# Optimization experiments

Measured on AMD Instinct MI355X. Metric: run time of the kernel, lower is better.

## Reference

```python
import jax, jax.numpy as jnp
import numpy as np

EPS = 1e-12  # torch F.normalize eps


def setup_inputs() -> dict:
    key = jax.random.key(0)
    k1, k2, k3 = jax.random.split(key, 3)
    B, D, H, W, K = 64, 512, 32, 32, 64
    x = jax.random.normal(k1, (B, D, H, W), dtype=jnp.float32)
    w = jax.random.normal(k2, (K, D), dtype=jnp.float32) * 0.05  # 1x1 conv weight
    c = jax.random.normal(k3, (K, D), dtype=jnp.float32)          # cluster centers
    return {"x": x, "w": w, "c": c}


def reference(x, w, c):
    B, D, H, W = x.shape
    K = w.shape[0]
    N = H * W
    # 1x1 conv (no bias): (B,D,H,W) x (K,D) -> (B,K,H,W)
    features = jnp.einsum('bdhw,kd->bkhw', x, w)
    # NOTE: original applies softmax over dim=2 (the H axis only)
    a_bar = jax.nn.softmax(features, axis=2)
    xf = x.reshape(B, D, N)
    a = a_bar.reshape(B, K, N)
    # V[b,k,d] = sum_n a[b,k,n] * (x[b,d,n] - c[k,d])
    V = jnp.einsum('bkn,bdn->bkd', a, xf) - a.sum(axis=2)[:, :, None] * c[None]
    V = V.transpose(2, 1, 0)  # (D, K, B)
    # F.normalize(V, p=2, dim=1) applied twice (second is idempotent)
    norm = jnp.maximum(jnp.linalg.norm(V, axis=1, keepdims=True), EPS)
    y = V / norm
    norm2 = jnp.maximum(jnp.linalg.norm(y, axis=1, keepdims=True), EPS)
    return y / norm2
```

## Files before the change

kernel.cpp:

```cpp
#include <hip/hip_runtime.h>


typedef __attribute__((ext_vector_type(8))) short short8;
typedef __attribute__((ext_vector_type(4))) float f32x4;
typedef unsigned short u16;
typedef unsigned int u32;

union S8u { u32 q[4]; short8 s; };

__device__ __forceinline__ u32 pk2(float lo, float hi) {
  union { float f; u32 u; } a, b; a.f = lo; b.f = hi;
  u32 xl = (a.u + 0x7fffu + ((a.u >> 16) & 1u)) >> 16;
  u32 xh = (b.u + 0x7fffu + ((b.u >> 16) & 1u)) & 0xffff0000u;
  return xl | xh;
}

typedef const __attribute__((address_space(1))) u32 GU32;
typedef __attribute__((address_space(3))) u32 LU32;
__device__ __forceinline__ void glds16(const void* g, void* l) {
  __builtin_amdgcn_global_load_lds((GU32*)g, (LU32*)l, 16, 0, 0);
}

__global__ __launch_bounds__(256) void k0_packw(
    const float* __restrict__ w, u16* __restrict__ wsw)
{
  const int tg = blockIdx.x * 256 + threadIdx.x;
  const int dd4 = tg & 7, i = (tg >> 3) & 15, k = tg >> 7;
  f32x4 v = *(const f32x4*)(w + k * 512 + i * 32 + dd4 * 4);
  u32* dst = (u32*)(wsw + (size_t)(i * 64 + k) * 32 + dd4 * 4);
  dst[0] = pk2(v[0], v[1]);
  dst[1] = pk2(v[2], v[3]);
}

__global__ __launch_bounds__(256, 3) void k1_features(
    const float* __restrict__ x, const u16* __restrict__ wsw,
    float* __restrict__ feat)
{
  const int blk = blockIdx.x;
  const int b = blk & 63, nt = blk >> 6;
  const int nb = nt * 64;
  const int tid = threadIdx.x, lane = tid & 63, wv = tid >> 6;
  const int row = lane & 15, q = lane >> 4;

  __shared__ __align__(16) float xs[4][32][64];

  const char* xbase = (const char*)(x + ((size_t)b << 19) + nb);
  const int r0 = tid >> 4, cb = (tid & 15) * 16;

  f32x4 acc[4];
#pragma unroll
  for (int mt = 0; mt < 4; mt++) acc[mt] = (f32x4){0.f, 0.f, 0.f, 0.f};

  short8 wf[4][4];

#define STAGE1(s)                                                              \
  {                                                                            \
    char* lx = (char*)&xs[(s) & 3][0][0];                                      \
    const char* gx = xbase + (size_t)(s) * 131072;                             \
    glds16(gx + (size_t)r0 * 4096 + cb, lx + r0 * 256 + cb);                   \
    glds16(gx + (size_t)(r0 + 16) * 4096 + cb, lx + (r0 + 16) * 256 + cb);     \
  }
#define LOADW(s)                                                               \
  {                                                                            \
    _Pragma("unroll")                                                          \
    for (int mt = 0; mt < 4; mt++)                                             \
      wf[(s) & 3][mt] = *(const short8*)(                                      \
          wsw + (size_t)(((s) * 64 + mt * 16 + row) * 32 + q * 8));            \
  }

  STAGE1(0); __builtin_amdgcn_sched_barrier(0);
  LOADW(0);  __builtin_amdgcn_sched_barrier(0);
  STAGE1(1); __builtin_amdgcn_sched_barrier(0);
  LOADW(1);  __builtin_amdgcn_sched_barrier(0);
  STAGE1(2); __builtin_amdgcn_sched_barrier(0);
  LOADW(2);  __builtin_amdgcn_sched_barrier(0);

#pragma unroll
  for (int i = 0; i < 16; i++) {
    if (i == 14)      asm volatile("s_waitcnt vmcnt(10)" ::: "memory");
    else if (i == 15) asm volatile("s_waitcnt vmcnt(4)" ::: "memory");
    else              asm volatile("s_waitcnt vmcnt(16)" ::: "memory");
    __builtin_amdgcn_s_barrier();
    __builtin_amdgcn_sched_barrier(0);
    if (i < 13) {
      STAGE1(i + 3); __builtin_amdgcn_sched_barrier(0);
      LOADW(i + 3);  __builtin_amdgcn_sched_barrier(0);
    }

    const float* xr = &xs[i & 3][0][wv * 16 + row];
    const int d8 = q * 8;
    float v0 = xr[(d8 + 0) * 64], v1 = xr[(d8 + 1) * 64];
    float v2 = xr[(d8 + 2) * 64], v3 = xr[(d8 + 3) * 64];
    float v4 = xr[(d8 + 4) * 64], v5 = xr[(d8 + 5) * 64];
    float v6 = xr[(d8 + 6) * 64], v7 = xr[(d8 + 7) * 64];
    S8u t;
    t.q[0] = pk2(v0, v1); t.q[1] = pk2(v2, v3);
    t.q[2] = pk2(v4, v5); t.q[3] = pk2(v6, v7);
    const short8 bfv = t.s;
#pragma unroll
    for (int mt = 0; mt < 4; mt++)
      acc[mt] = __builtin_amdgcn_mfma_f32_16x16x32_bf16(wf[i & 3][mt], bfv, acc[mt], 0, 0, 0);
  }
#undef STAGE1
#undef LOADW

  float* fb = feat + ((size_t)b << 16);
  const int nbw = nb + wv * 16 + row;
#pragma unroll
  for (int mt = 0; mt < 4; mt++)
#pragma unroll
    for (int r = 0; r < 4; r++)
      fb[(mt * 16 + q * 4 + r) * 1024 + nbw] = acc[mt][r];
}

__global__ __launch_bounds__(256) void k1b_softmax(
    const float* __restrict__ feat, u16* __restrict__ apad)
{
  const int tid = threadIdx.x, wv = tid >> 6, lane = tid & 63;
  const int rid = blockIdx.x * 4 + wv;
  const int b = rid >> 6, k = rid & 63;
  const float* f = feat + ((size_t)rid << 10);
  const int wl = (lane & 7) * 4;
  const int hq = lane >> 3;

  f32x4 v[4];
#pragma unroll
  for (int r = 0; r < 4; r++)
    v[r] = *(const f32x4*)(f + (hq + r * 8) * 32 + wl);

  f32x4 m = v[0];
#pragma unroll
  for (int r = 1; r < 4; r++)
#pragma unroll
    for (int c = 0; c < 4; c++) m[c] = fmaxf(m[c], v[r][c]);
#pragma unroll
  for (int mk = 8; mk <= 32; mk <<= 1)
#pragma unroll
    for (int c = 0; c < 4; c++) m[c] = fmaxf(m[c], __shfl_xor(m[c], mk));

  f32x4 s = (f32x4){0.f, 0.f, 0.f, 0.f};
#pragma unroll
  for (int r = 0; r < 4; r++)
#pragma unroll
    for (int c = 0; c < 4; c++) { v[r][c] = __expf(v[r][c] - m[c]); s[c] += v[r][c]; }
#pragma unroll
  for (int mk = 8; mk <= 32; mk <<= 1)
#pragma unroll
    for (int c = 0; c < 4; c++) s[c] += __shfl_xor(s[c], mk);

  f32x4 inv;
#pragma unroll
  for (int c = 0; c < 4; c++) inv[c] = 1.0f / s[c];

#pragma unroll
  for (int r = 0; r < 4; r++) {
    const int h = hq + r * 8;
    u32* dst = (u32*)(apad + ((size_t)(b * 32 + h) * 64 + k) * 32 + wl);
    dst[0] = pk2(v[r][0] * inv[0], v[r][1] * inv[1]);
    dst[1] = pk2(v[r][2] * inv[2], v[r][3] * inv[3]);
  }
}

__global__ __launch_bounds__(256, 2) void k2_aggregate(
    const float* __restrict__ x, const u16* __restrict__ apad,
    const float* __restrict__ cc, float* __restrict__ yw)
{
  const int blk = blockIdx.x;
  const int b = blk & 63, dt = blk >> 6;
  const int tid = threadIdx.x, lane = tid & 63, wv = tid >> 6;
  const int row = lane & 15, q = lane >> 4;

  const float* px0 = x + ((size_t)b << 19) + (size_t)(dt * 64 + wv * 16 + row) * 1024 + q * 8;
  const u16* ab = apad + ((size_t)b << 16) + (size_t)row * 32 + q * 8;

  f32x4 acc[4];
#pragma unroll
  for (int mt = 0; mt < 4; mt++) acc[mt] = (f32x4){0.f, 0.f, 0.f, 0.f};

  f32x4 xp0[4], xp1[4];
  short8 ap[3][4];
#pragma unroll
  for (int j = 0; j < 4; j++) {
    xp0[j] = *(const f32x4*)(px0 + j * 32);
    xp1[j] = *(const f32x4*)(px0 + j * 32 + 4);
  }
#pragma unroll
  for (int j = 0; j < 2; j++)
#pragma unroll
    for (int mt = 0; mt < 4; mt++)
      ap[j][mt] = *(const short8*)(ab + (size_t)j * 2048 + mt * 512);

#pragma unroll
  for (int i = 0; i < 32; i++) {
    const f32x4 c0 = xp0[i & 3], c1 = xp1[i & 3];
    S8u t;
    t.q[0] = pk2(c0[0], c0[1]); t.q[1] = pk2(c0[2], c0[3]);
    t.q[2] = pk2(c1[0], c1[1]); t.q[3] = pk2(c1[2], c1[3]);
    const short8 bfv = t.s;
#pragma unroll
    for (int mt = 0; mt < 4; mt++)
      acc[mt] = __builtin_amdgcn_mfma_f32_16x16x32_bf16(ap[i % 3][mt], bfv, acc[mt], 0, 0, 0);
    if (i + 4 < 32) {
      xp0[i & 3] = *(const f32x4*)(px0 + (i + 4) * 32);
      xp1[i & 3] = *(const f32x4*)(px0 + (i + 4) * 32 + 4);
    }
    if (i + 2 < 32) {
#pragma unroll
      for (int mt = 0; mt < 4; mt++)
        ap[(i + 2) % 3][mt] = *(const short8*)(ab + (size_t)(i + 2) * 2048 + mt * 512);
    }
  }

  const int dcol = dt * 64 + wv * 16 + row;
  float v[16]; float ss = 0.f;
#pragma unroll
  for (int mt = 0; mt < 4; mt++)
#pragma unroll
    for (int r = 0; r < 4; r++) {
      const int k = mt * 16 + q * 4 + r;
      const float tv = acc[mt][r] - 32.0f * cc[k * 512 + dcol];
      v[mt * 4 + r] = tv; ss += tv * tv;
    }
  ss += __shfl_xor(ss, 16);
  ss += __shfl_xor(ss, 32);
  const float rn = 1.0f / fmaxf(sqrtf(ss), 1e-12f);
  float* yb = yw + ((size_t)b << 15) + dcol;
#pragma unroll
  for (int mt = 0; mt < 4; mt++)
#pragma unroll
    for (int r = 0; r < 4; r++)
      yb[(size_t)(mt * 16 + q * 4 + r) << 9] = v[mt * 4 + r] * rn;
}

__global__ __launch_bounds__(256) void k3_transpose(
    const float* __restrict__ yw, float* __restrict__ out)
{
  const int blk = blockIdx.x;
  const int k = blk & 63;
  const int dt = blk >> 6;
  const int d0 = dt * 64;
  const int tid = threadIdx.x;
  __shared__ float T[64][68];
  {
    const int bl = tid >> 2, seg = tid & 3;
    const float* src = yw + (size_t)bl * 32768 + k * 512 + d0 + seg * 16;
#pragma unroll
    for (int i = 0; i < 4; i++) {
      f32x4 v = *(const f32x4*)(src + i * 4);
#pragma unroll
      for (int jj = 0; jj < 4; jj++) T[seg * 16 + i * 4 + jj][bl] = v[jj];
    }
  }
  __syncthreads();
  {
    const int dl = tid >> 2, bseg = tid & 3;
    float* dst = out + (size_t)(d0 + dl) * 4096 + k * 64 + bseg * 16;
    const float* srcT = &T[dl][bseg * 16];
#pragma unroll
    for (int i = 0; i < 4; i++)
      *(f32x4*)(dst + i * 4) = *(const f32x4*)(srcT + i * 4);
  }
}

extern "C" void kernel_launch(void* const* d_in, const int* in_sizes, int n_in,
                              void* d_out, int out_size, void* d_ws, size_t ws_size,
                              hipStream_t stream) {
  const float* x = (const float*)d_in[0];
  const float* w = (const float*)d_in[1];
  const float* c = (const float*)d_in[2];
  float* out = (float*)d_out;
  char* ws = (char*)d_ws;
  float* feat = (float*)ws;
  u16*   apad = (u16*)(ws + (size_t)16 * 1024 * 1024);
  float* yw   = (float*)(ws + (size_t)26 * 1024 * 1024);
  u16*   wsw  = (u16*)(ws + (size_t)34 * 1024 * 1024);
  k0_packw    <<<dim3(32),   dim3(256), 0, stream>>>(w, wsw);
  k1_features <<<dim3(1024), dim3(256), 0, stream>>>(x, wsw, feat);
  k1b_softmax <<<dim3(1024), dim3(256), 0, stream>>>(feat, apad);
  k2_aggregate<<<dim3(512),  dim3(256), 0, stream>>>(x, apad, c, yw);
  k3_transpose<<<dim3(512),  dim3(256), 0, stream>>>(yw, out);
}
```

Measured before the change: 242.8 us.

## Fuse 1x1-conv feature GEMM with H-axis softmax in one kernel

Merges the feature GEMM and the softmax over H into one kernel. Each 512-thread block computes all 32 H rows for an 8-wide W strip of one batch, so the softmax max and sum are reduced in LDS and the fp32 feature tensor never goes to global memory. The x staging tiles are re-laid out with an XOR swizzle and a 3-deep buffer, and one kernel launch is removed. In exchange the grid shrinks to 256 blocks at one block per CU, which lowers occupancy and latency hiding for the GEMM phase.

Measured after the change: 250.3 us. +3.1%, slower.

```diff
diff --git a/kernel.cpp b/kernel.cpp
--- a/kernel.cpp
+++ b/kernel.cpp
@@ -13,6 +13,11 @@
   u32 xl = (a.u + 0x7fffu + ((a.u >> 16) & 1u)) >> 16;
   u32 xh = (b.u + 0x7fffu + ((b.u >> 16) & 1u)) & 0xffff0000u;
   return xl | xh;
+}
+
+__device__ __forceinline__ u16 bf1(float f) {
+  union { float f; u32 u; } a; a.f = f;
+  return (u16)((a.u + 0x7fffu + ((a.u >> 16) & 1u)) >> 16);
 }
 
 typedef const __attribute__((address_space(1))) u32 GU32;
@@ -32,132 +37,165 @@
   dst[1] = pk2(v[2], v[3]);
 }
 
-__global__ __launch_bounds__(256, 3) void k1_features(
+__global__ __launch_bounds__(512, 1) void f1_feat_softmax(
     const float* __restrict__ x, const u16* __restrict__ wsw,
-    float* __restrict__ feat)
+    u16* __restrict__ apad)
 {
   const int blk = blockIdx.x;
-  const int b = blk & 63, nt = blk >> 6;
-  const int nb = nt * 64;
+  const int b = (blk & 7) | (((blk >> 3) & 7) << 3);
+  const int ws = blk >> 6;
   const int tid = threadIdx.x, lane = tid & 63, wv = tid >> 6;
-  const int row = lane & 15, q = lane >> 4;
-
-  __shared__ __align__(16) float xs[4][32][64];
-
-  const char* xbase = (const char*)(x + ((size_t)b << 19) + nb);
-  const int r0 = tid >> 4, cb = (tid & 15) * 16;
-
-  f32x4 acc[4];
-#pragma unroll
-  for (int mt = 0; mt < 4; mt++) acc[mt] = (f32x4){0.f, 0.f, 0.f, 0.f};
+  const int cc = lane & 15, q = lane >> 4;
+  const int wo = cc & 7, hh = cc >> 3;
+
+  __shared__ __align__(16) char smem[96 * 1024];
+
+  const char* xb = (const char*)(x + ((size_t)b << 19));
+
+  f32x4 acc[4][2];
+#pragma unroll
+  for (int mt = 0; mt < 4; mt++)
+#pragma unroll
+    for (int nt = 0; nt < 2; nt++) acc[mt][nt] = (f32x4){0.f, 0.f, 0.f, 0.f};
 
   short8 wf[4][4];
 
-#define STAGE1(s)                                                              \
+#define STAGEX(s)                                                              \
   {                                                                            \
-    char* lx = (char*)&xs[(s) & 3][0][0];                                      \
-    const char* gx = xbase + (size_t)(s) * 131072;                             \
-    glds16(gx + (size_t)r0 * 4096 + cb, lx + r0 * 256 + cb);                   \
-    glds16(gx + (size_t)(r0 + 16) * 4096 + cb, lx + (r0 + 16) * 256 + cb);     \
-  }
-#define LOADW(s)                                                               \
+    char* lb = smem + ((s) % 3) * 32768;                                       \
+    _Pragma("unroll")                                                          \
+    for (int j = 0; j < 4; j++) {                                              \
+      const int csrc = lane ^ (j << 2);                                        \
+      glds16(xb + (size_t)((s) * 32 + wv + 8 * j) * 4096                       \
+                 + (csrc >> 1) * 128 + ws * 32 + (csrc & 1) * 16,              \
+             lb + (wv + 8 * j) * 1024 + lane * 16);                            \
+    }                                                                          \
+  }
+#define LOADWF(s)                                                              \
   {                                                                            \
     _Pragma("unroll")                                                          \
     for (int mt = 0; mt < 4; mt++)                                             \
       wf[(s) & 3][mt] = *(const short8*)(                                      \
-          wsw + (size_t)(((s) * 64 + mt * 16 + row) * 32 + q * 8));            \
-  }
-
-  STAGE1(0); __builtin_amdgcn_sched_barrier(0);
-  LOADW(0);  __builtin_amdgcn_sched_barrier(0);
-  STAGE1(1); __builtin_amdgcn_sched_barrier(0);
-  LOADW(1);  __builtin_amdgcn_sched_barrier(0);
-  STAGE1(2); __builtin_amdgcn_sched_barrier(0);
-  LOADW(2);  __builtin_amdgcn_sched_barrier(0);
+          wsw + (size_t)(((s) * 64 + mt * 16 + cc) * 32 + q * 8));             \
+  }
+
+  LOADWF(0); __builtin_amdgcn_sched_barrier(0);
+  STAGEX(0); __builtin_amdgcn_sched_barrier(0);
+  LOADWF(1); __builtin_amdgcn_sched_barrier(0);
+  STAGEX(1); __builtin_amdgcn_sched_barrier(0);
 
 #pragma unroll
   for (int i = 0; i < 16; i++) {
-    if (i == 14)      asm volatile("s_waitcnt vmcnt(10)" ::: "memory");
-    else if (i == 15) asm volatile("s_waitcnt vmcnt(4)" ::: "memory");
-    else              asm volatile("s_waitcnt vmcnt(16)" ::: "memory");
+    if (i == 15) asm volatile("s_waitcnt vmcnt(0)" ::: "memory");
+    else         asm volatile("s_waitcnt vmcnt(8)" ::: "memory");
     __builtin_amdgcn_s_barrier();
     __builtin_amdgcn_sched_barrier(0);
-    if (i < 13) {
-      STAGE1(i + 3); __builtin_amdgcn_sched_barrier(0);
-      LOADW(i + 3);  __builtin_amdgcn_sched_barrier(0);
-    }
-
-    const float* xr = &xs[i & 3][0][wv * 16 + row];
-    const int d8 = q * 8;
-    float v0 = xr[(d8 + 0) * 64], v1 = xr[(d8 + 1) * 64];
-    float v2 = xr[(d8 + 2) * 64], v3 = xr[(d8 + 3) * 64];
-    float v4 = xr[(d8 + 4) * 64], v5 = xr[(d8 + 5) * 64];
-    float v6 = xr[(d8 + 6) * 64], v7 = xr[(d8 + 7) * 64];
-    S8u t;
-    t.q[0] = pk2(v0, v1); t.q[1] = pk2(v2, v3);
-    t.q[2] = pk2(v4, v5); t.q[3] = pk2(v6, v7);
-    const short8 bfv = t.s;
+    if (i < 14) {
+      LOADWF(i + 2); __builtin_amdgcn_sched_barrier(0);
+      STAGEX(i + 2); __builtin_amdgcn_sched_barrier(0);
+    }
+
+    const float* xsb = (const float*)(smem + (i % 3) * 32768);
+    short8 bfv[2];
+#pragma unroll
+    for (int nt = 0; nt < 2; nt++) {
+      const int colx = (wv * 32 + nt * 16 + cc) ^ (q << 4);
+      const float* xc = xsb + colx;
+      const int d0 = q * 8;
+      float v0 = xc[(d0 + 0) * 256], v1 = xc[(d0 + 1) * 256];
+      float v2 = xc[(d0 + 2) * 256], v3 = xc[(d0 + 3) * 256];
+      float v4 = xc[(d0 + 4) * 256], v5 = xc[(d0 + 5) * 256];
+      float v6 = xc[(d0 + 6) * 256], v7 = xc[(d0 + 7) * 256];
+      S8u t;
+      t.q[0] = pk2(v0, v1); t.q[1] = pk2(v2, v3);
+      t.q[2] = pk2(v4, v5); t.q[3] = pk2(v6, v7);
+      bfv[nt] = t.s;
+    }
+#pragma unroll
+    for (int nt = 0; nt < 2; nt++)
+#pragma unroll
+      for (int mt = 0; mt < 4; mt++)
+        acc[mt][nt] = __builtin_amdgcn_mfma_f32_16x16x32_bf16(wf[i & 3][mt], bfv[nt], acc[mt][nt], 0, 0, 0);
+  }
+#undef STAGEX
+#undef LOADWF
+
+  __syncthreads();
+  float* scr = (float*)smem;
+  u16* alds = (u16*)(smem + 20 * 1024);
+
+  float red[4][4];
+#pragma unroll
+  for (int mt = 0; mt < 4; mt++)
+#pragma unroll
+    for (int r = 0; r < 4; r++) {
+      float pm = fmaxf(acc[mt][0][r], acc[mt][1][r]);
+      pm = fmaxf(pm, __shfl_xor(pm, 8));
+      red[mt][r] = pm;
+    }
+  if (hh == 0) {
 #pragma unroll
     for (int mt = 0; mt < 4; mt++)
-      acc[mt] = __builtin_amdgcn_mfma_f32_16x16x32_bf16(wf[i & 3][mt], bfv, acc[mt], 0, 0, 0);
-  }
-#undef STAGE1
-#undef LOADW
-
-  float* fb = feat + ((size_t)b << 16);
-  const int nbw = nb + wv * 16 + row;
-#pragma unroll
-  for (int mt = 0; mt < 4; mt++)
-#pragma unroll
-    for (int r = 0; r < 4; r++)
-      fb[(mt * 16 + q * 4 + r) * 1024 + nbw] = acc[mt][r];
-}
-
-__global__ __launch_bounds__(256) void k1b_softmax(
-    const float* __restrict__ feat, u16* __restrict__ apad)
-{
-  const int tid = threadIdx.x, wv = tid >> 6, lane = tid & 63;
-  const int rid = blockIdx.x * 4 + wv;
-  const int b = rid >> 6, k = rid & 63;
-  const float* f = feat + ((size_t)rid << 10);
-  const int wl = (lane & 7) * 4;
-  const int hq = lane >> 3;
-
-  f32x4 v[4];
-#pragma unroll
-  for (int r = 0; r < 4; r++)
-    v[r] = *(const f32x4*)(f + (hq + r * 8) * 32 + wl);
-
-  f32x4 m = v[0];
-#pragma unroll
-  for (int r = 1; r < 4; r++)
-#pragma unroll
-    for (int c = 0; c < 4; c++) m[c] = fmaxf(m[c], v[r][c]);
-#pragma unroll
-  for (int mk = 8; mk <= 32; mk <<= 1)
-#pragma unroll
-    for (int c = 0; c < 4; c++) m[c] = fmaxf(m[c], __shfl_xor(m[c], mk));
-
-  f32x4 s = (f32x4){0.f, 0.f, 0.f, 0.f};
-#pragma unroll
-  for (int r = 0; r < 4; r++)
-#pragma unroll
-    for (int c = 0; c < 4; c++) { v[r][c] = __expf(v[r][c] - m[c]); s[c] += v[r][c]; }
-#pragma unroll
-  for (int mk = 8; mk <= 32; mk <<= 1)
-#pragma unroll
-    for (int c = 0; c < 4; c++) s[c] += __shfl_xor(s[c], mk);
-
-  f32x4 inv;
-#pragma unroll
-  for (int c = 0; c < 4; c++) inv[c] = 1.0f / s[c];
-
-#pragma unroll
-  for (int r = 0; r < 4; r++) {
-    const int h = hq + r * 8;
-    u32* dst = (u32*)(apad + ((size_t)(b * 32 + h) * 64 + k) * 32 + wl);
-    dst[0] = pk2(v[r][0] * inv[0], v[r][1] * inv[1]);
-    dst[1] = pk2(v[r][2] * inv[2], v[r][3] * inv[3]);
+#pragma unroll
+      for (int r = 0; r < 4; r++)
+        scr[((mt * 16 + q * 4 + r) * 8 + wo) * 9 + wv] = red[mt][r];
+  }
+  __syncthreads();
+  float mx[4][4];
+#pragma unroll
+  for (int mt = 0; mt < 4; mt++)
+#pragma unroll
+    for (int r = 0; r < 4; r++) {
+      const float* p = scr + ((mt * 16 + q * 4 + r) * 8 + wo) * 9;
+      float m0 = fmaxf(fmaxf(p[0], p[1]), fmaxf(p[2], p[3]));
+      float m1 = fmaxf(fmaxf(p[4], p[5]), fmaxf(p[6], p[7]));
+      mx[mt][r] = fmaxf(m0, m1);
+    }
+  __syncthreads();
+#pragma unroll
+  for (int mt = 0; mt < 4; mt++)
+#pragma unroll
+    for (int r = 0; r < 4; r++) {
+      float p0 = __expf(acc[mt][0][r] - mx[mt][r]);
+      float p1 = __expf(acc[mt][1][r] - mx[mt][r]);
+      acc[mt][0][r] = p0; acc[mt][1][r] = p1;
+      float ps = p0 + p1;
+      ps += __shfl_xor(ps, 8);
+      red[mt][r] = ps;
+    }
+  if (hh == 0) {
+#pragma unroll
+    for (int mt = 0; mt < 4; mt++)
+#pragma unroll
+      for (int r = 0; r < 4; r++)
+        scr[((mt * 16 + q * 4 + r) * 8 + wo) * 9 + wv] = red[mt][r];
+  }
+  __syncthreads();
+  float inv[4][4];
+#pragma unroll
+  for (int mt = 0; mt < 4; mt++)
+#pragma unroll
+    for (int r = 0; r < 4; r++) {
+      const float* p = scr + ((mt * 16 + q * 4 + r) * 8 + wo) * 9;
+      float s8 = ((p[0] + p[1]) + (p[2] + p[3])) + ((p[4] + p[5]) + (p[6] + p[7]));
+      inv[mt][r] = 1.0f / s8;
+    }
+#pragma unroll
+  for (int mt = 0; mt < 4; mt++)
+#pragma unroll
+    for (int nt = 0; nt < 2; nt++)
+#pragma unroll
+      for (int r = 0; r < 4; r++) {
+        const int h = wv * 4 + nt * 2 + hh;
+        const int kk = mt * 16 + q * 4 + r;
+        alds[(h * 64 + kk) * 8 + wo] = bf1(acc[mt][nt][r] * inv[mt][r]);
+      }
+  __syncthreads();
+  u16* ab = apad + ((size_t)b << 16) + ws * 8;
+#pragma unroll
+  for (int i = 0; i < 4; i++) {
+    const int idx = tid + i * 512;
+    *(f32x4*)(ab + (size_t)idx * 32) = *(const f32x4*)(alds + (size_t)idx * 8);
   }
 }
 
@@ -270,13 +308,11 @@
   const float* c = (const float*)d_in[2];
   float* out = (float*)d_out;
   char* ws = (char*)d_ws;
-  float* feat = (float*)ws;
   u16*   apad = (u16*)(ws + (size_t)16 * 1024 * 1024);
   float* yw   = (float*)(ws + (size_t)26 * 1024 * 1024);
   u16*   wsw  = (u16*)(ws + (size_t)34 * 1024 * 1024);
-  k0_packw    <<<dim3(32),   dim3(256), 0, stream>>>(w, wsw);
-  k1_features <<<dim3(1024), dim3(256), 0, stream>>>(x, wsw, feat);
-  k1b_softmax <<<dim3(1024), dim3(256), 0, stream>>>(feat, apad);
-  k2_aggregate<<<dim3(512),  dim3(256), 0, stream>>>(x, apad, c, yw);
-  k3_transpose<<<dim3(512),  dim3(256), 0, stream>>>(yw, out);
-}
+  k0_packw       <<<dim3(32),  dim3(256), 0, stream>>>(w, wsw);
+  f1_feat_softmax<<<dim3(256), dim3(512), 0, stream>>>(x, wsw, apad);
+  k2_aggregate   <<<dim3(512), dim3(256), 0, stream>>>(x, apad, c, yw);
+  k3_transpose   <<<dim3(512), dim3(256), 0, stream>>>(yw, out);
+}
```
